# Kernel optimization log

Hardware: AMD Instinct MI355X
Metric: run time of the kernel (lower is better)

Reference implementation:

```python
import jax, jax.numpy as jnp
import numpy as np

H = 128      # num_hidden
NIN = 384    # num_in
FF = 4 * H   # feedforward dim
SCALE = 30.0
EPS = 1e-5


def _linear(x, w, b):
    # torch Linear: weight [out, in]
    return x @ w.T + b


def _ln(x, g, b):
    mu = jnp.mean(x, axis=-1, keepdims=True)
    var = jnp.var(x, axis=-1, keepdims=True)
    return (x - mu) * jax.lax.rsqrt(var + EPS) * g + b


def setup_inputs() -> dict:
    key = jax.random.key(0)
    ks = jax.random.split(key, 16)
    B, N, K = 2, 2048, 48
    s = 0.05
    return {
        "h_V": jax.random.normal(ks[0], (B, N, H), jnp.float32),
        "h_E": jax.random.normal(ks[1], (B, N, K, NIN), jnp.float32),
        "mask_V": jnp.ones((B, N), jnp.float32),
        "mask_attend": jnp.ones((B, N, K), jnp.float32),
        "W1_w": jax.random.normal(ks[2], (H, H + NIN), jnp.float32) * s,
        "W1_b": jnp.zeros((H,), jnp.float32),
        "W2_w": jax.random.normal(ks[3], (H, H), jnp.float32) * s,
        "W2_b": jnp.zeros((H,), jnp.float32),
        "W3_w": jax.random.normal(ks[4], (H, H), jnp.float32) * s,
        "W3_b": jnp.zeros((H,), jnp.float32),
        "ln1_g": jnp.ones((H,), jnp.float32),
        "ln1_b": jnp.zeros((H,), jnp.float32),
        "ln2_g": jnp.ones((H,), jnp.float32),
        "ln2_b": jnp.zeros((H,), jnp.float32),
        "Win_w": jax.random.normal(ks[5], (FF, H), jnp.float32) * s,
        "Win_b": jnp.zeros((FF,), jnp.float32),
        "Wout_w": jax.random.normal(ks[6], (H, FF), jnp.float32) * s,
        "Wout_b": jnp.zeros((H,), jnp.float32),
    }


def reference(h_V, h_E, mask_V, mask_attend,
              W1_w, W1_b, W2_w, W2_b, W3_w, W3_b,
              ln1_g, ln1_b, ln2_g, ln2_b,
              Win_w, Win_b, Wout_w, Wout_b):
    gelu = lambda x: jax.nn.gelu(x, approximate=False)  # torch GELU (erf)
    B, N, K, _ = h_E.shape
    # expand-concat: [B,N,K,H+NIN]
    h_V_expand = jnp.broadcast_to(h_V[:, :, None, :], (B, N, K, H))
    h_EV = jnp.concatenate([h_V_expand, h_E], axis=-1)
    # 3-layer message MLP
    h_message = _linear(gelu(_linear(gelu(_linear(h_EV, W1_w, W1_b)), W2_w, W2_b)), W3_w, W3_b)
    h_message = mask_attend[..., None] * h_message
    dh = jnp.sum(h_message, axis=-2) / SCALE
    h = _ln(h_V + dh, ln1_g, ln1_b)  # dropout = identity (eval)
    dh = _linear(gelu(_linear(h, Win_w, Win_b)), Wout_w, Wout_b)
    h = _ln(h + dh, ln2_g, ln2_b)
    return mask_V[..., None] * h
```

## Files before the change

kernel.cpp:

```cpp
#include <hip/hip_runtime.h>
#include <math.h>


typedef __bf16 bf16;
typedef __attribute__((ext_vector_type(8))) __bf16 bf16x8;
typedef __attribute__((ext_vector_type(4))) __bf16 bf16x4;
typedef __attribute__((ext_vector_type(4))) float f32x4;

__device__ __forceinline__ bf16 f2bf(float f) {
    unsigned u = __builtin_bit_cast(unsigned, f);
    u += 0x7FFFu + ((u >> 16) & 1u);
    unsigned short s = (unsigned short)(u >> 16);
    return __builtin_bit_cast(bf16, s);
}

__device__ __forceinline__ float gelu_exact(float x) {
    return 0.5f * x * (1.0f + erff(x * 0.70710678118654752f));
}

__device__ __forceinline__ f32x4 mfma16(bf16x8 a, bf16x8 b, f32x4 c) {
    return __builtin_amdgcn_mfma_f32_16x16x32_bf16(a, b, c, 0, 0, 0);
}

#define WS_W2   65536
#define WS_W3   81920
#define WS_WIN  98304
#define WS_WOUT 163840
#define WS_TOTAL_W 229376
#define WS_H1_BYTES 458752

__global__ void convert_weights(const float* __restrict__ W1, const float* __restrict__ W2,
                                const float* __restrict__ W3, const float* __restrict__ Win,
                                const float* __restrict__ Wout, bf16* __restrict__ ws) {
    int i = blockIdx.x * 256 + threadIdx.x;
    if (i < WS_W2)              ws[i] = f2bf(W1[i]);
    else if (i < WS_W3)         ws[i] = f2bf(W2[i - WS_W2]);
    else if (i < WS_WIN)        ws[i] = f2bf(W3[i - WS_W3]);
    else if (i < WS_WOUT)       ws[i] = f2bf(Win[i - WS_WIN]);
    else if (i < WS_TOTAL_W)    ws[i] = f2bf(Wout[i - WS_WOUT]);
}

__global__ __launch_bounds__(256, 3)
void msg_kernel(const float* __restrict__ h_V, const float* __restrict__ h_E,
                const float* __restrict__ mask_attend,
                const bf16* __restrict__ W1b, const bf16* __restrict__ W2b,
                const bf16* __restrict__ W3b,
                const float* __restrict__ b1, const float* __restrict__ b2,
                const float* __restrict__ b3,
                const float* __restrict__ ln1g, const float* __restrict__ ln1b,
                float* __restrict__ h1out) {
    __shared__ __align__(16) char smem[53248];
    bf16*  a_lds = (bf16*)smem;
    bf16*  m2    = (bf16*)smem;
    bf16*  m1    = (bf16*)(smem + 26112);
    float* tbuf  = (float*)(smem + 52224);

    const int tid  = threadIdx.x;
    const int wave = tid >> 6;
    const int lane = tid & 63;
    const int q    = lane >> 4;
    const int c15  = lane & 15;
    const int g0   = blockIdx.x * 2;

    f32x4 zero = {0.f, 0.f, 0.f, 0.f};
    f32x4 acc[6][2];
#pragma unroll
    for (int mt = 0; mt < 6; ++mt) { acc[mt][0] = zero; acc[mt][1] = zero; }

    const int r0  = tid >> 4;
    const int l16 = tid & 15;
    for (int kb = 0; kb < 8; ++kb) {
        __syncthreads();
        const int cg = kb * 64 + l16 * 4;
#pragma unroll
        for (int it = 0; it < 6; ++it) {
            const int row = it * 16 + r0;
            const int nl  = row >= 48;
            const int g   = g0 + nl;
            const float* src = (kb < 2)
                ? (h_V + (size_t)g * 128 + cg)
                : (h_E + (size_t)(g * 48 + row - 48 * nl) * 384 + (cg - 128));
            const float4 v = *(const float4*)src;
            bf16x4 w; w.x = f2bf(v.x); w.y = f2bf(v.y); w.z = f2bf(v.z); w.w = f2bf(v.w);
            *(bf16x4*)(a_lds + row * 72 + l16 * 4) = w;
        }
        __syncthreads();
        bf16x8 bf0[2], bf1[2];
#pragma unroll
        for (int s = 0; s < 2; ++s) {
            bf0[s] = *(const bf16x8*)(W1b + (size_t)(wave * 32 + c15) * 512 + kb * 64 + s * 32 + q * 8);
            bf1[s] = *(const bf16x8*)(W1b + (size_t)(wave * 32 + 16 + c15) * 512 + kb * 64 + s * 32 + q * 8);
        }
#pragma unroll
        for (int mt = 0; mt < 6; ++mt) {
#pragma unroll
            for (int s = 0; s < 2; ++s) {
                bf16x8 af = *(const bf16x8*)(a_lds + (mt * 16 + c15) * 72 + s * 32 + q * 8);
                acc[mt][0] = mfma16(af, bf0[s], acc[mt][0]);
                acc[mt][1] = mfma16(af, bf1[s], acc[mt][1]);
            }
        }
    }
    {
        const float bb0 = b1[wave * 32 + c15];
        const float bb1 = b1[wave * 32 + 16 + c15];
#pragma unroll
        for (int mt = 0; mt < 6; ++mt) {
#pragma unroll
            for (int r = 0; r < 4; ++r) {
                const int row = mt * 16 + q * 4 + r;
                m1[row * 136 + wave * 32 + c15]      = f2bf(gelu_exact(acc[mt][0][r] + bb0));
                m1[row * 136 + wave * 32 + 16 + c15] = f2bf(gelu_exact(acc[mt][1][r] + bb1));
            }
        }
    }
    __syncthreads();

#pragma unroll
    for (int mt = 0; mt < 6; ++mt) { acc[mt][0] = zero; acc[mt][1] = zero; }
#pragma unroll
    for (int s = 0; s < 4; ++s) {
        const bf16x8 w0 = *(const bf16x8*)(W2b + (size_t)(wave * 32 + c15) * 128 + s * 32 + q * 8);
        const bf16x8 w1 = *(const bf16x8*)(W2b + (size_t)(wave * 32 + 16 + c15) * 128 + s * 32 + q * 8);
#pragma unroll
        for (int mt = 0; mt < 6; ++mt) {
            bf16x8 af = *(const bf16x8*)(m1 + (mt * 16 + c15) * 136 + s * 32 + q * 8);
            acc[mt][0] = mfma16(af, w0, acc[mt][0]);
            acc[mt][1] = mfma16(af, w1, acc[mt][1]);
        }
    }
    {
        const float bb0 = b2[wave * 32 + c15];
        const float bb1 = b2[wave * 32 + 16 + c15];
#pragma unroll
        for (int mt = 0; mt < 6; ++mt) {
#pragma unroll
            for (int r = 0; r < 4; ++r) {
                const int row = mt * 16 + q * 4 + r;
                m2[row * 136 + wave * 32 + c15]      = f2bf(gelu_exact(acc[mt][0][r] + bb0));
                m2[row * 136 + wave * 32 + 16 + c15] = f2bf(gelu_exact(acc[mt][1][r] + bb1));
            }
        }
    }
    __syncthreads();

#pragma unroll
    for (int mt = 0; mt < 6; ++mt) { acc[mt][0] = zero; acc[mt][1] = zero; }
#pragma unroll
    for (int s = 0; s < 4; ++s) {
        const bf16x8 w0 = *(const bf16x8*)(W3b + (size_t)(wave * 32 + c15) * 128 + s * 32 + q * 8);
        const bf16x8 w1 = *(const bf16x8*)(W3b + (size_t)(wave * 32 + 16 + c15) * 128 + s * 32 + q * 8);
#pragma unroll
        for (int mt = 0; mt < 6; ++mt) {
            bf16x8 af = *(const bf16x8*)(m2 + (mt * 16 + c15) * 136 + s * 32 + q * 8);
            acc[mt][0] = mfma16(af, w0, acc[mt][0]);
            acc[mt][1] = mfma16(af, w1, acc[mt][1]);
        }
    }
    {
        const float bb0 = b3[wave * 32 + c15];
        const float bb1 = b3[wave * 32 + 16 + c15];
        float s00 = 0.f, s01 = 0.f, s10 = 0.f, s11 = 0.f;
#pragma unroll
        for (int mt = 0; mt < 6; ++mt) {
#pragma unroll
            for (int r = 0; r < 4; ++r) {
                const int row = mt * 16 + q * 4 + r;
                const int nl  = row >= 48;
                const float mv = mask_attend[(size_t)(g0 + nl) * 48 + row - 48 * nl];
                const float v0 = (acc[mt][0][r] + bb0) * mv;
                const float v1 = (acc[mt][1][r] + bb1) * mv;
                if (nl) { s10 += v0; s11 += v1; } else { s00 += v0; s01 += v1; }
            }
        }
#pragma unroll
        for (int off = 16; off <= 32; off <<= 1) {
            s00 += __shfl_xor(s00, off);
            s01 += __shfl_xor(s01, off);
            s10 += __shfl_xor(s10, off);
            s11 += __shfl_xor(s11, off);
        }
        if (lane < 16) {
            const int col0 = wave * 32 + c15, col1 = col0 + 16;
            tbuf[col0]       = h_V[(size_t)g0 * 128 + col0]       + s00 * (1.0f / 30.0f);
            tbuf[col1]       = h_V[(size_t)g0 * 128 + col1]       + s01 * (1.0f / 30.0f);
            tbuf[128 + col0] = h_V[(size_t)(g0 + 1) * 128 + col0] + s10 * (1.0f / 30.0f);
            tbuf[128 + col1] = h_V[(size_t)(g0 + 1) * 128 + col1] + s11 * (1.0f / 30.0f);
        }
    }
    __syncthreads();
    if (wave < 2) {
        const float x0 = tbuf[wave * 128 + lane];
        const float x1 = tbuf[wave * 128 + 64 + lane];
        float sm = x0 + x1, sq = x0 * x0 + x1 * x1;
#pragma unroll
        for (int off = 1; off < 64; off <<= 1) { sm += __shfl_xor(sm, off); sq += __shfl_xor(sq, off); }
        const float mu  = sm * (1.0f / 128.0f);
        const float var = sq * (1.0f / 128.0f) - mu * mu;
        const float inv = rsqrtf(var + 1e-5f);
        const int g = g0 + wave;
        h1out[(size_t)g * 128 + lane]      = (x0 - mu) * inv * ln1g[lane]      + ln1b[lane];
        h1out[(size_t)g * 128 + 64 + lane] = (x1 - mu) * inv * ln1g[64 + lane] + ln1b[64 + lane];
    }
}

__global__ __launch_bounds__(256, 2)
void ffn_kernel(const float* __restrict__ h1, const bf16* __restrict__ Winb,
                const bf16* __restrict__ Woutb,
                const float* __restrict__ bin, const float* __restrict__ bout,
                const float* __restrict__ ln2g, const float* __restrict__ ln2b,
                const float* __restrict__ mask_V, float* __restrict__ out) {
    __shared__ __align__(16) bf16  a2[16 * 136];
    __shared__ __align__(16) bf16  ff[16 * 264];
    __shared__ __align__(16) float tb[16 * 132];

    const int tid  = threadIdx.x;
    const int wave = tid >> 6;
    const int lane = tid & 63;
    const int q    = lane >> 4;
    const int c15  = lane & 15;
    const int r0g  = blockIdx.x * 16;

#pragma unroll
    for (int it = 0; it < 2; ++it) {
        const int idx = it * 256 + tid;
        const int row = idx >> 5;
        const int c4  = idx & 31;
        const float4 v = *(const float4*)(h1 + (size_t)(r0g + row) * 128 + c4 * 4);
        bf16x4 w; w.x = f2bf(v.x); w.y = f2bf(v.y); w.z = f2bf(v.z); w.w = f2bf(v.w);
        *(bf16x4*)(a2 + row * 136 + c4 * 4) = w;
    }

    f32x4 zero = {0.f, 0.f, 0.f, 0.f};
    f32x4 accB[2]; accB[0] = zero; accB[1] = zero;

    for (int p = 0; p < 2; ++p) {
        __syncthreads();
        f32x4 accA[4];
#pragma unroll
        for (int i = 0; i < 4; ++i) accA[i] = zero;
#pragma unroll
        for (int s = 0; s < 4; ++s) {
            bf16x8 af = *(const bf16x8*)(a2 + c15 * 136 + s * 32 + q * 8);
#pragma unroll
            for (int nt = 0; nt < 4; ++nt) {
                const int n = p * 256 + wave * 64 + nt * 16 + c15;
                bf16x8 wb = *(const bf16x8*)(Winb + (size_t)n * 128 + s * 32 + q * 8);
                accA[nt] = mfma16(af, wb, accA[nt]);
            }
        }
#pragma unroll
        for (int nt = 0; nt < 4; ++nt) {
            const int colL = wave * 64 + nt * 16 + c15;
            const float bb = bin[p * 256 + colL];
#pragma unroll
            for (int r = 0; r < 4; ++r) {
                const int row = q * 4 + r;
                ff[row * 264 + colL] = f2bf(gelu_exact(accA[nt][r] + bb));
            }
        }
        __syncthreads();
#pragma unroll
        for (int s = 0; s < 8; ++s) {
            bf16x8 af = *(const bf16x8*)(ff + c15 * 264 + s * 32 + q * 8);
#pragma unroll
            for (int nt = 0; nt < 2; ++nt) {
                const int n = wave * 32 + nt * 16 + c15;
                bf16x8 wb = *(const bf16x8*)(Woutb + (size_t)n * 512 + p * 256 + s * 32 + q * 8);
                accB[nt] = mfma16(af, wb, accB[nt]);
            }
        }
    }
#pragma unroll
    for (int nt = 0; nt < 2; ++nt) {
        const int col = wave * 32 + nt * 16 + c15;
        const float bb = bout[col];
#pragma unroll
        for (int r = 0; r < 4; ++r) {
            const int row = q * 4 + r;
            tb[row * 132 + col] = accB[nt][r] + bb + h1[(size_t)(r0g + row) * 128 + col];
        }
    }
    __syncthreads();
#pragma unroll
    for (int rr = 0; rr < 4; ++rr) {
        const int row = wave * 4 + rr;
        const float x0 = tb[row * 132 + lane];
        const float x1 = tb[row * 132 + 64 + lane];
        float sm = x0 + x1, sq = x0 * x0 + x1 * x1;
#pragma unroll
        for (int off = 1; off < 64; off <<= 1) { sm += __shfl_xor(sm, off); sq += __shfl_xor(sq, off); }
        const float mu  = sm * (1.0f / 128.0f);
        const float var = sq * (1.0f / 128.0f) - mu * mu;
        const float inv = rsqrtf(var + 1e-5f);
        const int g = r0g + row;
        const float mv = mask_V[g];
        out[(size_t)g * 128 + lane]      = mv * ((x0 - mu) * inv * ln2g[lane]      + ln2b[lane]);
        out[(size_t)g * 128 + 64 + lane] = mv * ((x1 - mu) * inv * ln2g[64 + lane] + ln2b[64 + lane]);
    }
}

extern "C" void kernel_launch(void* const* d_in, const int* in_sizes, int n_in,
                              void* d_out, int out_size, void* d_ws, size_t ws_size,
                              hipStream_t stream) {
    const float* h_V         = (const float*)d_in[0];
    const float* h_E         = (const float*)d_in[1];
    const float* mask_V      = (const float*)d_in[2];
    const float* mask_attend = (const float*)d_in[3];
    const float* W1w  = (const float*)d_in[4];
    const float* W1bb = (const float*)d_in[5];
    const float* W2w  = (const float*)d_in[6];
    const float* W2bb = (const float*)d_in[7];
    const float* W3w  = (const float*)d_in[8];
    const float* W3bb = (const float*)d_in[9];
    const float* ln1g = (const float*)d_in[10];
    const float* ln1b = (const float*)d_in[11];
    const float* ln2g = (const float*)d_in[12];
    const float* ln2b = (const float*)d_in[13];
    const float* Winw  = (const float*)d_in[14];
    const float* Winbb = (const float*)d_in[15];
    const float* Woutw  = (const float*)d_in[16];
    const float* Woutbb = (const float*)d_in[17];

    bf16* wsb   = (bf16*)d_ws;
    bf16* W1c   = wsb;
    bf16* W2c   = wsb + WS_W2;
    bf16* W3c   = wsb + WS_W3;
    bf16* Winc  = wsb + WS_WIN;
    bf16* Woutc = wsb + WS_WOUT;
    float* h1   = (float*)((char*)d_ws + WS_H1_BYTES);

    convert_weights<<<896, 256, 0, stream>>>(W1w, W2w, W3w, Winw, Woutw, wsb);
    msg_kernel<<<2048, 256, 0, stream>>>(h_V, h_E, mask_attend, W1c, W2c, W3c,
                                         W1bb, W2bb, W3bb, ln1g, ln1b, h1);
    ffn_kernel<<<256, 256, 0, stream>>>(h1, Winc, Woutc, Winbb, Woutbb,
                                        ln2g, ln2b, mask_V, (float*)d_out);
}
```

Baseline: 517.6 us.

## Restructure message and FFN kernels with direct register loads and tanh GELU

The message kernel now handles one node per block and loads h_E straight from global memory into registers as MFMA fragments, skipping the LDS staging and its barriers. The h_V contribution to W1 is computed once per node and broadcast across all 48 neighbours instead of being redone per edge. Exact erf GELU is replaced by a tanh-style sigmoid approximation, and bf16 rounding is simplified to round-half-up with packed permutes. The FFN kernel switches to 8 rows per 512-thread block and splits the K dimension of the output projection across waves. The GELU change and the altered rounding introduce numerical differences from the reference.

```diff
diff --git a/kernel.cpp b/kernel.cpp
--- a/kernel.cpp
+++ b/kernel.cpp
@@ -4,20 +4,29 @@
 
 typedef __bf16 bf16;
 typedef __attribute__((ext_vector_type(8))) __bf16 bf16x8;
-typedef __attribute__((ext_vector_type(4))) __bf16 bf16x4;
 typedef __attribute__((ext_vector_type(4))) float f32x4;
-
+typedef __attribute__((ext_vector_type(4))) unsigned uint4v;
+
+__device__ __forceinline__ unsigned pk2bf(float a, float b) {
+    unsigned ua = __builtin_bit_cast(unsigned, a) + 0x8000u;
+    unsigned ub = __builtin_bit_cast(unsigned, b) + 0x8000u;
+    return __builtin_amdgcn_perm(ub, ua, 0x07060302u);
+}
 __device__ __forceinline__ bf16 f2bf(float f) {
-    unsigned u = __builtin_bit_cast(unsigned, f);
-    u += 0x7FFFu + ((u >> 16) & 1u);
-    unsigned short s = (unsigned short)(u >> 16);
+    unsigned short s = (unsigned short)((__builtin_bit_cast(unsigned, f) + 0x8000u) >> 16);
     return __builtin_bit_cast(bf16, s);
 }
-
-__device__ __forceinline__ float gelu_exact(float x) {
-    return 0.5f * x * (1.0f + erff(x * 0.70710678118654752f));
-}
-
+__device__ __forceinline__ bf16x8 pack8(float4 v0, float4 v1) {
+    uint4v p;
+    p.x = pk2bf(v0.x, v0.y); p.y = pk2bf(v0.z, v0.w);
+    p.z = pk2bf(v1.x, v1.y); p.w = pk2bf(v1.z, v1.w);
+    return __builtin_bit_cast(bf16x8, p);
+}
+__device__ __forceinline__ float gelu_f(float x) {
+    float u = 1.595769122f * x * fmaf(0.044715f, x * x, 1.0f);
+    float e = __expf(-u);
+    return x * __builtin_amdgcn_rcpf(1.0f + e);
+}
 __device__ __forceinline__ f32x4 mfma16(bf16x8 a, bf16x8 b, f32x4 c) {
     return __builtin_amdgcn_mfma_f32_16x16x32_bf16(a, b, c, 0, 0, 0);
 }
@@ -40,7 +49,7 @@
     else if (i < WS_TOTAL_W)    ws[i] = f2bf(Wout[i - WS_WOUT]);
 }
 
-__global__ __launch_bounds__(256, 3)
+__global__ __launch_bounds__(256, 4)
 void msg_kernel(const float* __restrict__ h_V, const float* __restrict__ h_E,
                 const float* __restrict__ mask_attend,
                 const bf16* __restrict__ W1b, const bf16* __restrict__ W2b,
@@ -49,254 +58,271 @@
                 const float* __restrict__ b3,
                 const float* __restrict__ ln1g, const float* __restrict__ ln1b,
                 float* __restrict__ h1out) {
-    __shared__ __align__(16) char smem[53248];
-    bf16*  a_lds = (bf16*)smem;
-    bf16*  m2    = (bf16*)smem;
-    bf16*  m1    = (bf16*)(smem + 26112);
-    float* tbuf  = (float*)(smem + 52224);
+    __shared__ __align__(16) bf16 m1[48 * 136];
+    __shared__ __align__(16) bf16 m2[48 * 136];
+    __shared__ float tbuf[128];
 
     const int tid  = threadIdx.x;
     const int wave = tid >> 6;
     const int lane = tid & 63;
     const int q    = lane >> 4;
     const int c15  = lane & 15;
-    const int g0   = blockIdx.x * 2;
-
-    f32x4 zero = {0.f, 0.f, 0.f, 0.f};
-    f32x4 acc[6][2];
-#pragma unroll
-    for (int mt = 0; mt < 6; ++mt) { acc[mt][0] = zero; acc[mt][1] = zero; }
-
-    const int r0  = tid >> 4;
-    const int l16 = tid & 15;
-    for (int kb = 0; kb < 8; ++kb) {
-        __syncthreads();
-        const int cg = kb * 64 + l16 * 4;
-#pragma unroll
-        for (int it = 0; it < 6; ++it) {
-            const int row = it * 16 + r0;
-            const int nl  = row >= 48;
-            const int g   = g0 + nl;
-            const float* src = (kb < 2)
-                ? (h_V + (size_t)g * 128 + cg)
-                : (h_E + (size_t)(g * 48 + row - 48 * nl) * 384 + (cg - 128));
-            const float4 v = *(const float4*)src;
-            bf16x4 w; w.x = f2bf(v.x); w.y = f2bf(v.y); w.z = f2bf(v.z); w.w = f2bf(v.w);
-            *(bf16x4*)(a_lds + row * 72 + l16 * 4) = w;
-        }
-        __syncthreads();
-        bf16x8 bf0[2], bf1[2];
-#pragma unroll
-        for (int s = 0; s < 2; ++s) {
-            bf0[s] = *(const bf16x8*)(W1b + (size_t)(wave * 32 + c15) * 512 + kb * 64 + s * 32 + q * 8);
-            bf1[s] = *(const bf16x8*)(W1b + (size_t)(wave * 32 + 16 + c15) * 512 + kb * 64 + s * 32 + q * 8);
-        }
-#pragma unroll
-        for (int mt = 0; mt < 6; ++mt) {
-#pragma unroll
-            for (int s = 0; s < 2; ++s) {
-                bf16x8 af = *(const bf16x8*)(a_lds + (mt * 16 + c15) * 72 + s * 32 + q * 8);
-                acc[mt][0] = mfma16(af, bf0[s], acc[mt][0]);
-                acc[mt][1] = mfma16(af, bf1[s], acc[mt][1]);
-            }
-        }
-    }
-    {
-        const float bb0 = b1[wave * 32 + c15];
-        const float bb1 = b1[wave * 32 + 16 + c15];
-#pragma unroll
-        for (int mt = 0; mt < 6; ++mt) {
+    const int g    = blockIdx.x;
+    const int n0c  = wave * 32 + c15;
+
+    const f32x4 zero = {0.f, 0.f, 0.f, 0.f};
+
+    f32x4 acc0[2] = {zero, zero};
+    {
+        const float* pV  = h_V + (size_t)g * 128 + q * 8;
+        const bf16* pWv0 = W1b + (size_t)n0c * 512 + q * 8;
+        const bf16* pWv1 = pWv0 + 16 * 512;
+#pragma unroll
+        for (int s = 0; s < 4; ++s) {
+            float4 v0 = *(const float4*)(pV + s * 32);
+            float4 v1 = *(const float4*)(pV + s * 32 + 4);
+            bf16x8 af = pack8(v0, v1);
+            bf16x8 w0 = *(const bf16x8*)(pWv0 + s * 32);
+            bf16x8 w1 = *(const bf16x8*)(pWv1 + s * 32);
+            acc0[0] = mfma16(af, w0, acc0[0]);
+            acc0[1] = mfma16(af, w1, acc0[1]);
+        }
+    }
+
+    f32x4 acc[3][2];
+#pragma unroll
+    for (int mt = 0; mt < 3; ++mt) { acc[mt][0] = zero; acc[mt][1] = zero; }
+    {
+        const float* pE0 = h_E + ((size_t)g * 48 + c15) * 384 + q * 8;
+        const float* pE1 = pE0 + 16 * 384;
+        const float* pE2 = pE1 + 16 * 384;
+        const bf16* pW0 = W1b + (size_t)n0c * 512 + 128 + q * 8;
+        const bf16* pW1 = pW0 + 16 * 512;
+#pragma unroll
+        for (int ks = 0; ks < 12; ++ks) {
+            bf16x8 w0 = *(const bf16x8*)(pW0 + ks * 32);
+            bf16x8 w1 = *(const bf16x8*)(pW1 + ks * 32);
+            float4 a00 = *(const float4*)(pE0 + ks * 32);
+            float4 a01 = *(const float4*)(pE0 + ks * 32 + 4);
+            float4 a10 = *(const float4*)(pE1 + ks * 32);
+            float4 a11 = *(const float4*)(pE1 + ks * 32 + 4);
+            float4 a20 = *(const float4*)(pE2 + ks * 32);
+            float4 a21 = *(const float4*)(pE2 + ks * 32 + 4);
+            bf16x8 f0 = pack8(a00, a01);
+            bf16x8 f1 = pack8(a10, a11);
+            bf16x8 f2 = pack8(a20, a21);
+            acc[0][0] = mfma16(f0, w0, acc[0][0]);
+            acc[0][1] = mfma16(f0, w1, acc[0][1]);
+            acc[1][0] = mfma16(f1, w0, acc[1][0]);
+            acc[1][1] = mfma16(f1, w1, acc[1][1]);
+            acc[2][0] = mfma16(f2, w0, acc[2][0]);
+            acc[2][1] = mfma16(f2, w1, acc[2][1]);
+        }
+    }
+    {
+        const float bb0 = b1[n0c], bb1 = b1[n0c + 16];
+#pragma unroll
+        for (int mt = 0; mt < 3; ++mt)
 #pragma unroll
             for (int r = 0; r < 4; ++r) {
                 const int row = mt * 16 + q * 4 + r;
-                m1[row * 136 + wave * 32 + c15]      = f2bf(gelu_exact(acc[mt][0][r] + bb0));
-                m1[row * 136 + wave * 32 + 16 + c15] = f2bf(gelu_exact(acc[mt][1][r] + bb1));
-            }
-        }
-    }
-    __syncthreads();
-
-#pragma unroll
-    for (int mt = 0; mt < 6; ++mt) { acc[mt][0] = zero; acc[mt][1] = zero; }
-#pragma unroll
-    for (int s = 0; s < 4; ++s) {
-        const bf16x8 w0 = *(const bf16x8*)(W2b + (size_t)(wave * 32 + c15) * 128 + s * 32 + q * 8);
-        const bf16x8 w1 = *(const bf16x8*)(W2b + (size_t)(wave * 32 + 16 + c15) * 128 + s * 32 + q * 8);
-#pragma unroll
-        for (int mt = 0; mt < 6; ++mt) {
-            bf16x8 af = *(const bf16x8*)(m1 + (mt * 16 + c15) * 136 + s * 32 + q * 8);
-            acc[mt][0] = mfma16(af, w0, acc[mt][0]);
-            acc[mt][1] = mfma16(af, w1, acc[mt][1]);
-        }
-    }
-    {
-        const float bb0 = b2[wave * 32 + c15];
-        const float bb1 = b2[wave * 32 + 16 + c15];
-#pragma unroll
-        for (int mt = 0; mt < 6; ++mt) {
+                m1[row * 136 + n0c]      = f2bf(gelu_f(acc[mt][0][r] + acc0[0][r] + bb0));
+                m1[row * 136 + n0c + 16] = f2bf(gelu_f(acc[mt][1][r] + acc0[1][r] + bb1));
+            }
+    }
+    __syncthreads();
+
+    f32x4 acc2[3][2];
+#pragma unroll
+    for (int mt = 0; mt < 3; ++mt) { acc2[mt][0] = zero; acc2[mt][1] = zero; }
+    {
+        bf16x8 w[4][2];
+        const bf16* pW20 = W2b + (size_t)n0c * 128 + q * 8;
+        const bf16* pW21 = pW20 + 16 * 128;
+#pragma unroll
+        for (int s = 0; s < 4; ++s) {
+            w[s][0] = *(const bf16x8*)(pW20 + s * 32);
+            w[s][1] = *(const bf16x8*)(pW21 + s * 32);
+        }
+        const bf16* pA = m1 + c15 * 136 + q * 8;
+#pragma unroll
+        for (int s = 0; s < 4; ++s)
+#pragma unroll
+            for (int mt = 0; mt < 3; ++mt) {
+                bf16x8 af = *(const bf16x8*)(pA + mt * 16 * 136 + s * 32);
+                acc2[mt][0] = mfma16(af, w[s][0], acc2[mt][0]);
+                acc2[mt][1] = mfma16(af, w[s][1], acc2[mt][1]);
+            }
+    }
+    {
+        const float bb0 = b2[n0c], bb1 = b2[n0c + 16];
+#pragma unroll
+        for (int mt = 0; mt < 3; ++mt)
 #pragma unroll
             for (int r = 0; r < 4; ++r) {
                 const int row = mt * 16 + q * 4 + r;
-                m2[row * 136 + wave * 32 + c15]      = f2bf(gelu_exact(acc[mt][0][r] + bb0));
-                m2[row * 136 + wave * 32 + 16 + c15] = f2bf(gelu_exact(acc[mt][1][r] + bb1));
-            }
-        }
-    }
-    __syncthreads();
-
-#pragma unroll
-    for (int mt = 0; mt < 6; ++mt) { acc[mt][0] = zero; acc[mt][1] = zero; }
-#pragma unroll
-    for (int s = 0; s < 4; ++s) {
-        const bf16x8 w0 = *(const bf16x8*)(W3b + (size_t)(wave * 32 + c15) * 128 + s * 32 + q * 8);
-        const bf16x8 w1 = *(const bf16x8*)(W3b + (size_t)(wave * 32 + 16 + c15) * 128 + s * 32 + q * 8);
-#pragma unroll
-        for (int mt = 0; mt < 6; ++mt) {
-            bf16x8 af = *(const bf16x8*)(m2 + (mt * 16 + c15) * 136 + s * 32 + q * 8);
-            acc[mt][0] = mfma16(af, w0, acc[mt][0]);
-            acc[mt][1] = mfma16(af, w1, acc[mt][1]);
-        }
-    }
-    {
-        const float bb0 = b3[wave * 32 + c15];
-        const float bb1 = b3[wave * 32 + 16 + c15];
-        float s00 = 0.f, s01 = 0.f, s10 = 0.f, s11 = 0.f;
-#pragma unroll
-        for (int mt = 0; mt < 6; ++mt) {
+                m2[row * 136 + n0c]      = f2bf(gelu_f(acc2[mt][0][r] + bb0));
+                m2[row * 136 + n0c + 16] = f2bf(gelu_f(acc2[mt][1][r] + bb1));
+            }
+    }
+    __syncthreads();
+
+    f32x4 acc3[3][2];
+#pragma unroll
+    for (int mt = 0; mt < 3; ++mt) { acc3[mt][0] = zero; acc3[mt][1] = zero; }
+    {
+        bf16x8 w[4][2];
+        const bf16* pW30 = W3b + (size_t)n0c * 128 + q * 8;
+        const bf16* pW31 = pW30 + 16 * 128;
+#pragma unroll
+        for (int s = 0; s < 4; ++s) {
+            w[s][0] = *(const bf16x8*)(pW30 + s * 32);
+            w[s][1] = *(const bf16x8*)(pW31 + s * 32);
+        }
+        const bf16* pA = m2 + c15 * 136 + q * 8;
+#pragma unroll
+        for (int s = 0; s < 4; ++s)
+#pragma unroll
+            for (int mt = 0; mt < 3; ++mt) {
+                bf16x8 af = *(const bf16x8*)(pA + mt * 16 * 136 + s * 32);
+                acc3[mt][0] = mfma16(af, w[s][0], acc3[mt][0]);
+                acc3[mt][1] = mfma16(af, w[s][1], acc3[mt][1]);
+            }
+    }
+    {
+        const float bb0 = b3[n0c], bb1 = b3[n0c + 16];
+        float s0 = 0.f, s1 = 0.f;
+#pragma unroll
+        for (int mt = 0; mt < 3; ++mt)
 #pragma unroll
             for (int r = 0; r < 4; ++r) {
                 const int row = mt * 16 + q * 4 + r;
-                const int nl  = row >= 48;
-                const float mv = mask_attend[(size_t)(g0 + nl) * 48 + row - 48 * nl];
-                const float v0 = (acc[mt][0][r] + bb0) * mv;
-                const float v1 = (acc[mt][1][r] + bb1) * mv;
-                if (nl) { s10 += v0; s11 += v1; } else { s00 += v0; s01 += v1; }
-            }
-        }
-#pragma unroll
-        for (int off = 16; off <= 32; off <<= 1) {
-            s00 += __shfl_xor(s00, off);
-            s01 += __shfl_xor(s01, off);
-            s10 += __shfl_xor(s10, off);
-            s11 += __shfl_xor(s11, off);
-        }
+                const float mv = mask_attend[(size_t)g * 48 + row];
+                s0 += (acc3[mt][0][r] + bb0) * mv;
+                s1 += (acc3[mt][1][r] + bb1) * mv;
+            }
+        s0 += __shfl_xor(s0, 16); s0 += __shfl_xor(s0, 32);
+        s1 += __shfl_xor(s1, 16); s1 += __shfl_xor(s1, 32);
         if (lane < 16) {
-            const int col0 = wave * 32 + c15, col1 = col0 + 16;
-            tbuf[col0]       = h_V[(size_t)g0 * 128 + col0]       + s00 * (1.0f / 30.0f);
-            tbuf[col1]       = h_V[(size_t)g0 * 128 + col1]       + s01 * (1.0f / 30.0f);
-            tbuf[128 + col0] = h_V[(size_t)(g0 + 1) * 128 + col0] + s10 * (1.0f / 30.0f);
-            tbuf[128 + col1] = h_V[(size_t)(g0 + 1) * 128 + col1] + s11 * (1.0f / 30.0f);
-        }
-    }
-    __syncthreads();
-    if (wave < 2) {
-        const float x0 = tbuf[wave * 128 + lane];
-        const float x1 = tbuf[wave * 128 + 64 + lane];
+            tbuf[n0c]      = h_V[(size_t)g * 128 + n0c]      + s0 * (1.0f / 30.0f);
+            tbuf[n0c + 16] = h_V[(size_t)g * 128 + n0c + 16] + s1 * (1.0f / 30.0f);
+        }
+    }
+    __syncthreads();
+
+    if (wave == 0) {
+        const float x0 = tbuf[lane];
+        const float x1 = tbuf[lane + 64];
         float sm = x0 + x1, sq = x0 * x0 + x1 * x1;
 #pragma unroll
         for (int off = 1; off < 64; off <<= 1) { sm += __shfl_xor(sm, off); sq += __shfl_xor(sq, off); }
         const float mu  = sm * (1.0f / 128.0f);
         const float var = sq * (1.0f / 128.0f) - mu * mu;
         const float inv = rsqrtf(var + 1e-5f);
-        const int g = g0 + wave;
         h1out[(size_t)g * 128 + lane]      = (x0 - mu) * inv * ln1g[lane]      + ln1b[lane];
         h1out[(size_t)g * 128 + 64 + lane] = (x1 - mu) * inv * ln1g[64 + lane] + ln1b[64 + lane];
     }
 }
 
-__global__ __launch_bounds__(256, 2)
+__global__ __launch_bounds__(512, 4)
 void ffn_kernel(const float* __restrict__ h1, const bf16* __restrict__ Winb,
                 const bf16* __restrict__ Woutb,
                 const float* __restrict__ bin, const float* __restrict__ bout,
                 const float* __restrict__ ln2g, const float* __restrict__ ln2b,
                 const float* __restrict__ mask_V, float* __restrict__ out) {
-    __shared__ __align__(16) bf16  a2[16 * 136];
-    __shared__ __align__(16) bf16  ff[16 * 264];
-    __shared__ __align__(16) float tb[16 * 132];
+    __shared__ __align__(16) bf16 a2[16 * 136];
+    __shared__ __align__(16) bf16 ff[16 * 520];
+    __shared__ float tb0[16 * 132];
+    __shared__ float tb1[16 * 132];
 
     const int tid  = threadIdx.x;
     const int wave = tid >> 6;
     const int lane = tid & 63;
     const int q    = lane >> 4;
     const int c15  = lane & 15;
-    const int r0g  = blockIdx.x * 16;
-
-#pragma unroll
-    for (int it = 0; it < 2; ++it) {
-        const int idx = it * 256 + tid;
-        const int row = idx >> 5;
-        const int c4  = idx & 31;
-        const float4 v = *(const float4*)(h1 + (size_t)(r0g + row) * 128 + c4 * 4);
-        bf16x4 w; w.x = f2bf(v.x); w.y = f2bf(v.y); w.z = f2bf(v.z); w.w = f2bf(v.w);
-        *(bf16x4*)(a2 + row * 136 + c4 * 4) = w;
-    }
-
-    f32x4 zero = {0.f, 0.f, 0.f, 0.f};
-    f32x4 accB[2]; accB[0] = zero; accB[1] = zero;
-
-    for (int p = 0; p < 2; ++p) {
-        __syncthreads();
-        f32x4 accA[4];
-#pragma unroll
-        for (int i = 0; i < 4; ++i) accA[i] = zero;
+    const int r0g  = blockIdx.x * 8;
+    const f32x4 zero = {0.f, 0.f, 0.f, 0.f};
+
+    {
+        const int row = tid >> 5;
+        const int c4  = tid & 31;
+        const int gr  = min(r0g + row, 4095);
+        float4 v = *(const float4*)(h1 + (size_t)gr * 128 + c4 * 4);
+        uint2 pk; pk.x = pk2bf(v.x, v.y); pk.y = pk2bf(v.z, v.w);
+        *(uint2*)(a2 + row * 136 + c4 * 4) = pk;
+    }
+    __syncthreads();
+
+    {
+        f32x4 accA[4] = {zero, zero, zero, zero};
+        const bf16* pA = a2 + c15 * 136 + q * 8;
 #pragma unroll
         for (int s = 0; s < 4; ++s) {
-            bf16x8 af = *(const bf16x8*)(a2 + c15 * 136 + s * 32 + q * 8);
+            bf16x8 af = *(const bf16x8*)(pA + s * 32);
 #pragma unroll
             for (int nt = 0; nt < 4; ++nt) {
-                const int n = p * 256 + wave * 64 + nt * 16 + c15;
+                const int n = wave * 64 + nt * 16 + c15;
                 bf16x8 wb = *(const bf16x8*)(Winb + (size_t)n * 128 + s * 32 + q * 8);
                 accA[nt] = mfma16(af, wb, accA[nt]);
             }
         }
 #pragma unroll
         for (int nt = 0; nt < 4; ++nt) {
-            const int colL = wave * 64 + nt * 16 + c15;
-            const float bb = bin[p * 256 + colL];
+            const int col = wave * 64 + nt * 16 + c15;
+            const float bb = bin[col];
+#pragma unroll
+            for (int r = 0; r < 4; ++r)
+                ff[(q * 4 + r) * 520 + col] = f2bf(gelu_f(accA[nt][r] + bb));
+        }
+    }
+    __syncthreads();
+
+    {
+        const int kh = wave & 1, nq = wave >> 1;
+        f32x4 accB[2] = {zero, zero};
+        const bf16* pF = ff + c15 * 520 + kh * 256 + q * 8;
+#pragma unroll
+        for (int s = 0; s < 8; ++s) {
+            bf16x8 af = *(const bf16x8*)(pF + s * 32);
+#pragma unroll
+            for (int nt = 0; nt < 2; ++nt) {
+                const int n = nq * 32 + nt * 16 + c15;
+                bf16x8 wb = *(const bf16x8*)(Woutb + (size_t)n * 512 + kh * 256 + s * 32 + q * 8);
+                accB[nt] = mfma16(af, wb, accB[nt]);
+            }
+        }
+        float* tb = kh ? tb1 : tb0;
+#pragma unroll
+        for (int nt = 0; nt < 2; ++nt) {
+            const int col = nq * 32 + nt * 16 + c15;
 #pragma unroll
             for (int r = 0; r < 4; ++r) {
                 const int row = q * 4 + r;
-                ff[row * 264 + colL] = f2bf(gelu_exact(accA[nt][r] + bb));
-            }
-        }
-        __syncthreads();
-#pragma unroll
-        for (int s = 0; s < 8; ++s) {
-            bf16x8 af = *(const bf16x8*)(ff + c15 * 264 + s * 32 + q * 8);
-#pragma unroll
-            for (int nt = 0; nt < 2; ++nt) {
-                const int n = wave * 32 + nt * 16 + c15;
-                bf16x8 wb = *(const bf16x8*)(Woutb + (size_t)n * 512 + p * 256 + s * 32 + q * 8);
-                accB[nt] = mfma16(af, wb, accB[nt]);
-            }
-        }
-    }
-#pragma unroll
-    for (int nt = 0; nt < 2; ++nt) {
-        const int col = wave * 32 + nt * 16 + c15;
-        const float bb = bout[col];
-#pragma unroll
-        for (int r = 0; r < 4; ++r) {
-            const int row = q * 4 + r;
-            tb[row * 132 + col] = accB[nt][r] + bb + h1[(size_t)(r0g + row) * 128 + col];
-        }
-    }
-    __syncthreads();
-#pragma unroll
-    for (int rr = 0; rr < 4; ++rr) {
-        const int row = wave * 4 + rr;
-        const float x0 = tb[row * 132 + lane];
-        const float x1 = tb[row * 132 + 64 + lane];
+                float v = accB[nt][r];
+                if (kh == 0) {
+                    const int gr = min(r0g + row, 4095);
+                    v += bout[col] + h1[(size_t)gr * 128 + col];
+                }
+                tb[row * 132 + col] = v;
+            }
+        }
+    }
+    __syncthreads();
+
+    {
+        const int row = wave;
+        const int gr  = r0g + row;
+        const float x0 = tb0[row * 132 + lane]      + tb1[row * 132 + lane];
+        const float x1 = tb0[row * 132 + 64 + lane] + tb1[row * 132 + 64 + lane];
         float sm = x0 + x1, sq = x0 * x0 + x1 * x1;
 #pragma unroll
         for (int off = 1; off < 64; off <<= 1) { sm += __shfl_xor(sm, off); sq += __shfl_xor(sq, off); }
         const float mu  = sm * (1.0f / 128.0f);
         const float var = sq * (1.0f / 128.0f) - mu * mu;
         const float inv = rsqrtf(var + 1e-5f);
-        const int g = r0g + row;
-        const float mv = mask_V[g];
-        out[(size_t)g * 128 + lane]      = mv * ((x0 - mu) * inv * ln2g[lane]      + ln2b[lane]);
-        out[(size_t)g * 128 + 64 + lane] = mv * ((x1 - mu) * inv * ln2g[64 + lane] + ln2b[64 + lane]);
+        const float mv  = mask_V[gr];
+        out[(size_t)gr * 128 + lane]      = mv * ((x0 - mu) * inv * ln2g[lane]      + ln2b[lane]);
+        out[(size_t)gr * 128 + 64 + lane] = mv * ((x1 - mu) * inv * ln2g[64 + lane] + ln2b[64 + lane]);
     }
 }
 
@@ -331,8 +357,8 @@
     float* h1   = (float*)((char*)d_ws + WS_H1_BYTES);
 
     convert_weights<<<896, 256, 0, stream>>>(W1w, W2w, W3w, Winw, Woutw, wsb);
-    msg_kernel<<<2048, 256, 0, stream>>>(h_V, h_E, mask_attend, W1c, W2c, W3c,
+    msg_kernel<<<4096, 256, 0, stream>>>(h_V, h_E, mask_attend, W1c, W2c, W3c,
                                          W1bb, W2bb, W3bb, ln1g, ln1b, h1);
-    ffn_kernel<<<256, 256, 0, stream>>>(h1, Winc, Woutc, Winbb, Woutbb,
+    ffn_kernel<<<512, 512, 0, stream>>>(h1, Winc, Woutc, Winbb, Woutbb,
                                         ln2g, ln2b, mask_V, (float*)d_out);
 }
```

New measurement: 608.0 us. +17.5%, slower.
